# Kernel optimization log

Hardware: AMD Instinct MI355X
Metric: run time of the kernel (lower is better)

Reference implementation:

```python
import jax, jax.numpy as jnp
from jax import lax
import numpy as np

S, B, T = 512, 256, 128


def setup_inputs() -> dict:
    key = jax.random.key(0)
    k1, k2, k3, k4 = jax.random.split(key, 4)
    emissions = jax.random.normal(k1, (S, B, T), dtype=jnp.float32)
    mask = jnp.ones((S, B), dtype=jnp.int32)  # all positions valid
    start_transitions = jax.random.normal(k2, (T,), dtype=jnp.float32)
    end_transitions = jax.random.normal(k3, (T,), dtype=jnp.float32)
    transitions = jax.random.normal(k4, (T, T), dtype=jnp.float32)
    return {
        "emissions": emissions,
        "mask": mask,
        "start_transitions": start_transitions,
        "end_transitions": end_transitions,
        "transitions": transitions,
    }


def reference(emissions, mask, start_transitions, end_transitions, transitions):
    """Viterbi decode. emissions: [S,B,T], mask: [S,B].
    Returns (best_tags [B,S] int32, best_path_score [B] float32)."""
    seq_len, batch, num_tags = emissions.shape
    maskb = mask.astype(bool)

    score0 = start_transitions[None, :] + emissions[0]  # [B,T]

    def fwd_step(score, inp):
        em_t, m_t = inp  # [B,T], [B]
        # [B, T_prev, T_next]
        ns = score[:, :, None] + transitions[None, :, :] + em_t[:, None, :]
        next_score = ns.max(axis=1)          # [B,T]
        idx = ns.argmax(axis=1)              # [B,T] best previous tag
        score = jnp.where(m_t[:, None], next_score, score)
        return score, idx

    final_score, history = lax.scan(fwd_step, score0, (emissions[1:], maskb[1:]))
    final_score = final_score + end_transitions[None, :]

    best_last = jnp.argmax(final_score, axis=1)   # [B] tag at last valid position
    best_score = jnp.max(final_score, axis=1)     # [B]

    barange = jnp.arange(batch)

    def back_step(tag, inp):
        hist_t, m_t = inp  # [B,T], [B]
        prev = hist_t[barange, tag]
        tag = jnp.where(m_t, prev, tag)  # only follow history inside the sequence
        return tag, tag

    # reverse scan over transitions t -> t+1 for t = S-2 .. 0; ys[t] = tag at time t
    _, tags_prefix = lax.scan(back_step, best_last, (history, maskb[1:]), reverse=True)
    tags = jnp.concatenate([tags_prefix, best_last[None, :]], axis=0)  # [S,B]
    return tags.T.astype(jnp.int32), best_score
```

## Files before the change

kernel.cpp:

```cpp
#include <hip/hip_runtime.h>

#define SLEN  512
#define BATCH 256
#define NTAGS 128
#define NTHR  512

__device__ __forceinline__ int dpp_qperm_b1(int x) {
    return __builtin_amdgcn_update_dpp(0, x, 0xB1, 0xF, 0xF, true);
}
__device__ __forceinline__ int dpp_qperm_4e(int x) {
    return __builtin_amdgcn_update_dpp(0, x, 0x4E, 0xF, 0xF, true);
}

struct VI { float v; int i; };
__device__ __forceinline__ VI vmax2(VI a, VI b) { return (b.v > a.v) ? b : a; }

__global__ __launch_bounds__(NTHR, 2) void viterbi_kernel(
    const float* __restrict__ em,
    const int*   __restrict__ mask,
    const float* __restrict__ start_t,
    const float* __restrict__ end_t,
    const float* __restrict__ trans,
    float* __restrict__ out)
{
    const int b    = blockIdx.x;
    const int tid  = threadIdx.x;
    const int j    = tid >> 2;
    const int h    = tid & 3;
    const int base = h << 5;
    const bool writer = (h == 0);
    const int jslot = j + (j >> 5) * 8;

    __shared__ __align__(16) float scbuf[2][4 * 40];
    __shared__ float fin[NTAGS];
    __shared__ int   maskv[SLEN];
    __shared__ unsigned char hist[SLEN - 1][NTAGS];
    __shared__ unsigned char exitc[8][NTAGS];
    __shared__ unsigned char st_tags[8];
    __shared__ unsigned char tagseq[SLEN];
    __shared__ float bestval_s;
    __shared__ int   bestj_s;

    const float* trp = trans + (size_t)base * NTAGS + j;
    const float t00 = trp[ 0*NTAGS], t01 = trp[ 1*NTAGS], t02 = trp[ 2*NTAGS], t03 = trp[ 3*NTAGS];
    const float t04 = trp[ 4*NTAGS], t05 = trp[ 5*NTAGS], t06 = trp[ 6*NTAGS], t07 = trp[ 7*NTAGS];
    const float t08 = trp[ 8*NTAGS], t09 = trp[ 9*NTAGS], t10 = trp[10*NTAGS], t11 = trp[11*NTAGS];
    const float t12 = trp[12*NTAGS], t13 = trp[13*NTAGS], t14 = trp[14*NTAGS], t15 = trp[15*NTAGS];
    const float t16 = trp[16*NTAGS], t17 = trp[17*NTAGS], t18 = trp[18*NTAGS], t19 = trp[19*NTAGS];
    const float t20 = trp[20*NTAGS], t21 = trp[21*NTAGS], t22 = trp[22*NTAGS], t23 = trp[23*NTAGS];
    const float t24 = trp[24*NTAGS], t25 = trp[25*NTAGS], t26 = trp[26*NTAGS], t27 = trp[27*NTAGS];
    const float t28 = trp[28*NTAGS], t29 = trp[29*NTAGS], t30 = trp[30*NTAGS], t31 = trp[31*NTAGS];

    for (int t = tid; t < SLEN; t += NTHR)
        maskv[t] = mask[t * BATCH + b];

    float scj = 0.f;
    if (writer) {
        scj = start_t[j] + em[(size_t)b * NTAGS + j];
        scbuf[0][jslot] = scj;
    }
    __syncthreads();

    const float* emp = em + (size_t)BATCH * NTAGS + (size_t)b * NTAGS + j;
    float em_next = *emp;

    int p = 0;
    for (int t = 1; t < SLEN; ++t) {
        const float em_cur = em_next;
        if (t + 1 < SLEN) { emp += BATCH * NTAGS; em_next = *emp; }

        const float4* sq = (const float4*)&scbuf[p][h * 40];
        const float4 q0 = sq[0], q1 = sq[1], q2 = sq[2], q3 = sq[3];
        const float4 q4 = sq[4], q5 = sq[5], q6 = sq[6], q7 = sq[7];

        const float c00 = (q0.x + t00) + em_cur, c01 = (q0.y + t01) + em_cur;
        const float c02 = (q0.z + t02) + em_cur, c03 = (q0.w + t03) + em_cur;
        const float c04 = (q1.x + t04) + em_cur, c05 = (q1.y + t05) + em_cur;
        const float c06 = (q1.z + t06) + em_cur, c07 = (q1.w + t07) + em_cur;
        const float c08 = (q2.x + t08) + em_cur, c09 = (q2.y + t09) + em_cur;
        const float c10 = (q2.z + t10) + em_cur, c11 = (q2.w + t11) + em_cur;
        const float c12 = (q3.x + t12) + em_cur, c13 = (q3.y + t13) + em_cur;
        const float c14 = (q3.z + t14) + em_cur, c15 = (q3.w + t15) + em_cur;
        const float c16 = (q4.x + t16) + em_cur, c17 = (q4.y + t17) + em_cur;
        const float c18 = (q4.z + t18) + em_cur, c19 = (q4.w + t19) + em_cur;
        const float c20 = (q5.x + t20) + em_cur, c21 = (q5.y + t21) + em_cur;
        const float c22 = (q5.z + t22) + em_cur, c23 = (q5.w + t23) + em_cur;
        const float c24 = (q6.x + t24) + em_cur, c25 = (q6.y + t25) + em_cur;
        const float c26 = (q6.z + t26) + em_cur, c27 = (q6.w + t27) + em_cur;
        const float c28 = (q7.x + t28) + em_cur, c29 = (q7.y + t29) + em_cur;
        const float c30 = (q7.z + t30) + em_cur, c31 = (q7.w + t31) + em_cur;

        const VI m00 = vmax2(VI{c00, 0}, VI{c01, 1}),  m01 = vmax2(VI{c02, 2}, VI{c03, 3});
        const VI m02 = vmax2(VI{c04, 4}, VI{c05, 5}),  m03 = vmax2(VI{c06, 6}, VI{c07, 7});
        const VI m04 = vmax2(VI{c08, 8}, VI{c09, 9}),  m05 = vmax2(VI{c10,10}, VI{c11,11});
        const VI m06 = vmax2(VI{c12,12}, VI{c13,13}),  m07 = vmax2(VI{c14,14}, VI{c15,15});
        const VI m08 = vmax2(VI{c16,16}, VI{c17,17}),  m09 = vmax2(VI{c18,18}, VI{c19,19});
        const VI m10 = vmax2(VI{c20,20}, VI{c21,21}),  m11 = vmax2(VI{c22,22}, VI{c23,23});
        const VI m12 = vmax2(VI{c24,24}, VI{c25,25}),  m13 = vmax2(VI{c26,26}, VI{c27,27});
        const VI m14 = vmax2(VI{c28,28}, VI{c29,29}),  m15 = vmax2(VI{c30,30}, VI{c31,31});

        const VI n0 = vmax2(m00, m01), n1 = vmax2(m02, m03);
        const VI n2 = vmax2(m04, m05), n3 = vmax2(m06, m07);
        const VI n4 = vmax2(m08, m09), n5 = vmax2(m10, m11);
        const VI n6 = vmax2(m12, m13), n7 = vmax2(m14, m15);

        const VI o0 = vmax2(n0, n1), o1 = vmax2(n2, n3);
        const VI o2 = vmax2(n4, n5), o3 = vmax2(n6, n7);

        const VI p0 = vmax2(o0, o1), p1 = vmax2(o2, o3);
        const VI r  = vmax2(p0, p1);

        float v  = r.v;
        int   gi = base + r.i;
        {
            float vo = __int_as_float(dpp_qperm_b1(__float_as_int(v)));
            int   io = dpp_qperm_b1(gi);
            if (vo > v) { v = vo; gi = io; }
        }
        {
            float vo = __int_as_float(dpp_qperm_4e(__float_as_int(v)));
            int   io = dpp_qperm_4e(gi);
            if (vo > v) { v = vo; gi = io; }
        }

        if (writer) {
            hist[t - 1][j] = (unsigned char)gi;
            scj = maskv[t] ? v : scj;
            scbuf[p ^ 1][jslot] = scj;
        }
        __syncthreads();
        p ^= 1;
    }

    if (writer) fin[j] = scj + end_t[j];
    __syncthreads();

    if (tid < 64) {
        float v  = fin[tid]; int bj = tid;
        float v1 = fin[tid + 64];
        if (v1 > v) { v = v1; bj = tid + 64; }
#pragma unroll
        for (int off = 32; off > 0; off >>= 1) {
            float ov = __shfl_xor(v, off, 64);
            int   oj = __shfl_xor(bj, off, 64);
            if (ov > v || (ov == v && oj < bj)) { v = ov; bj = oj; }
        }
        if (tid == 0) { bestval_s = v; bestj_s = bj; }
    }
    __syncthreads();

    {
        const int k  = tid & 127;
        const int c0 = tid >> 7;
        const int c1 = c0 + 4;
        int tagA = k, tagB = k;
        for (int u = 63; u >= 0; --u) {
            const int sA = c0 * 64 + u;
            const int sB = c1 * 64 + u;
            if (sB <= SLEN - 2) {
                int pv = hist[sB][tagB];
                tagB = maskv[sB + 1] ? pv : tagB;
            }
            int pv = hist[sA][tagA];
            tagA = maskv[sA + 1] ? pv : tagA;
        }
        exitc[c0][k] = (unsigned char)tagA;
        exitc[c1][k] = (unsigned char)tagB;
    }
    __syncthreads();

    if (tid == 0) {
        int tag = bestj_s;
        for (int c = 7; c >= 0; --c) {
            st_tags[c] = (unsigned char)tag;
            tag = exitc[c][tag];
        }
        out[BATCH * SLEN + b] = bestval_s;
    }
    __syncthreads();

    if (tid < 8) {
        const int c = tid;
        int tag = st_tags[c];
        if (c == 7) tagseq[SLEN - 1] = (unsigned char)tag;
        const int shi = (c == 7) ? (SLEN - 2) : (c * 64 + 63);
        for (int s = shi; s >= c * 64; --s) {
            int pv = hist[s][tag];
            tag = maskv[s + 1] ? pv : tag;
            tagseq[s] = (unsigned char)tag;
        }
    }
    __syncthreads();

    out[b * SLEN + tid] = (float)tagseq[tid];
}

extern "C" void kernel_launch(void* const* d_in, const int* in_sizes, int n_in,
                              void* d_out, int out_size, void* d_ws, size_t ws_size,
                              hipStream_t stream) {
    const float* em      = (const float*)d_in[0];
    const int*   mask    = (const int*)d_in[1];
    const float* start_t = (const float*)d_in[2];
    const float* end_t   = (const float*)d_in[3];
    const float* trans   = (const float*)d_in[4];
    float* out = (float*)d_out;

    viterbi_kernel<<<dim3(BATCH), dim3(NTHR), 0, stream>>>(
        em, mask, start_t, end_t, trans, out);
}
```

Measured before the change: 405.7 us.

## Split each tag's max-reduction across eight lanes with 1024-thread blocks

Doubles the block size to 1024 threads so each next-tag column is reduced by 8 lanes over 16 previous tags instead of 4 lanes over 32. A third butterfly step using ds_swizzle xor-4 finishes the reduction, and the shared score buffer padding is changed to match. The backtrace chunk walk is rebalanced to one chunk per thread. The goal is a shorter per-step serial dependency chain and fewer transition registers per thread. In exchange it adds an extra cross-lane step and doubles the number of waves that must meet at the per-step barrier.

```diff
diff --git a/kernel.cpp b/kernel.cpp
--- a/kernel.cpp
+++ b/kernel.cpp
@@ -3,7 +3,7 @@
 #define SLEN  512
 #define BATCH 256
 #define NTAGS 128
-#define NTHR  512
+#define NTHR  1024
 
 __device__ __forceinline__ int dpp_qperm_b1(int x) {
     return __builtin_amdgcn_update_dpp(0, x, 0xB1, 0xF, 0xF, true);
@@ -11,11 +11,14 @@
 __device__ __forceinline__ int dpp_qperm_4e(int x) {
     return __builtin_amdgcn_update_dpp(0, x, 0x4E, 0xF, 0xF, true);
 }
+__device__ __forceinline__ int swz_xor4(int x) {
+    return __builtin_amdgcn_ds_swizzle(x, 0x101F);
+}
 
 struct VI { float v; int i; };
 __device__ __forceinline__ VI vmax2(VI a, VI b) { return (b.v > a.v) ? b : a; }
 
-__global__ __launch_bounds__(NTHR, 2) void viterbi_kernel(
+__global__ __launch_bounds__(NTHR, 4) void viterbi_kernel(
     const float* __restrict__ em,
     const int*   __restrict__ mask,
     const float* __restrict__ start_t,
@@ -25,13 +28,13 @@
 {
     const int b    = blockIdx.x;
     const int tid  = threadIdx.x;
-    const int j    = tid >> 2;
-    const int h    = tid & 3;
-    const int base = h << 5;
+    const int j    = tid >> 3;
+    const int h    = tid & 7;
+    const int base = h << 4;
     const bool writer = (h == 0);
-    const int jslot = j + (j >> 5) * 8;
+    const int jslot = j + (j >> 4) * 4;
 
-    __shared__ __align__(16) float scbuf[2][4 * 40];
+    __shared__ __align__(16) float scbuf[2][8 * 20];
     __shared__ float fin[NTAGS];
     __shared__ int   maskv[SLEN];
     __shared__ unsigned char hist[SLEN - 1][NTAGS];
@@ -46,13 +49,9 @@
     const float t04 = trp[ 4*NTAGS], t05 = trp[ 5*NTAGS], t06 = trp[ 6*NTAGS], t07 = trp[ 7*NTAGS];
     const float t08 = trp[ 8*NTAGS], t09 = trp[ 9*NTAGS], t10 = trp[10*NTAGS], t11 = trp[11*NTAGS];
     const float t12 = trp[12*NTAGS], t13 = trp[13*NTAGS], t14 = trp[14*NTAGS], t15 = trp[15*NTAGS];
-    const float t16 = trp[16*NTAGS], t17 = trp[17*NTAGS], t18 = trp[18*NTAGS], t19 = trp[19*NTAGS];
-    const float t20 = trp[20*NTAGS], t21 = trp[21*NTAGS], t22 = trp[22*NTAGS], t23 = trp[23*NTAGS];
-    const float t24 = trp[24*NTAGS], t25 = trp[25*NTAGS], t26 = trp[26*NTAGS], t27 = trp[27*NTAGS];
-    const float t28 = trp[28*NTAGS], t29 = trp[29*NTAGS], t30 = trp[30*NTAGS], t31 = trp[31*NTAGS];
 
-    for (int t = tid; t < SLEN; t += NTHR)
-        maskv[t] = mask[t * BATCH + b];
+    if (tid < SLEN)
+        maskv[tid] = mask[tid * BATCH + b];
 
     float scj = 0.f;
     if (writer) {
@@ -69,9 +68,8 @@
         const float em_cur = em_next;
         if (t + 1 < SLEN) { emp += BATCH * NTAGS; em_next = *emp; }
 
-        const float4* sq = (const float4*)&scbuf[p][h * 40];
+        const float4* sq = (const float4*)&scbuf[p][h * 20];
         const float4 q0 = sq[0], q1 = sq[1], q2 = sq[2], q3 = sq[3];
-        const float4 q4 = sq[4], q5 = sq[5], q6 = sq[6], q7 = sq[7];
 
         const float c00 = (q0.x + t00) + em_cur, c01 = (q0.y + t01) + em_cur;
         const float c02 = (q0.z + t02) + em_cur, c03 = (q0.w + t03) + em_cur;
@@ -81,34 +79,15 @@
         const float c10 = (q2.z + t10) + em_cur, c11 = (q2.w + t11) + em_cur;
         const float c12 = (q3.x + t12) + em_cur, c13 = (q3.y + t13) + em_cur;
         const float c14 = (q3.z + t14) + em_cur, c15 = (q3.w + t15) + em_cur;
-        const float c16 = (q4.x + t16) + em_cur, c17 = (q4.y + t17) + em_cur;
-        const float c18 = (q4.z + t18) + em_cur, c19 = (q4.w + t19) + em_cur;
-        const float c20 = (q5.x + t20) + em_cur, c21 = (q5.y + t21) + em_cur;
-        const float c22 = (q5.z + t22) + em_cur, c23 = (q5.w + t23) + em_cur;
-        const float c24 = (q6.x + t24) + em_cur, c25 = (q6.y + t25) + em_cur;
-        const float c26 = (q6.z + t26) + em_cur, c27 = (q6.w + t27) + em_cur;
-        const float c28 = (q7.x + t28) + em_cur, c29 = (q7.y + t29) + em_cur;
-        const float c30 = (q7.z + t30) + em_cur, c31 = (q7.w + t31) + em_cur;
 
-        const VI m00 = vmax2(VI{c00, 0}, VI{c01, 1}),  m01 = vmax2(VI{c02, 2}, VI{c03, 3});
-        const VI m02 = vmax2(VI{c04, 4}, VI{c05, 5}),  m03 = vmax2(VI{c06, 6}, VI{c07, 7});
-        const VI m04 = vmax2(VI{c08, 8}, VI{c09, 9}),  m05 = vmax2(VI{c10,10}, VI{c11,11});
-        const VI m06 = vmax2(VI{c12,12}, VI{c13,13}),  m07 = vmax2(VI{c14,14}, VI{c15,15});
-        const VI m08 = vmax2(VI{c16,16}, VI{c17,17}),  m09 = vmax2(VI{c18,18}, VI{c19,19});
-        const VI m10 = vmax2(VI{c20,20}, VI{c21,21}),  m11 = vmax2(VI{c22,22}, VI{c23,23});
-        const VI m12 = vmax2(VI{c24,24}, VI{c25,25}),  m13 = vmax2(VI{c26,26}, VI{c27,27});
-        const VI m14 = vmax2(VI{c28,28}, VI{c29,29}),  m15 = vmax2(VI{c30,30}, VI{c31,31});
-
-        const VI n0 = vmax2(m00, m01), n1 = vmax2(m02, m03);
-        const VI n2 = vmax2(m04, m05), n3 = vmax2(m06, m07);
-        const VI n4 = vmax2(m08, m09), n5 = vmax2(m10, m11);
-        const VI n6 = vmax2(m12, m13), n7 = vmax2(m14, m15);
-
+        const VI m0 = vmax2(VI{c00, 0}, VI{c01, 1}),  m1 = vmax2(VI{c02, 2}, VI{c03, 3});
+        const VI m2 = vmax2(VI{c04, 4}, VI{c05, 5}),  m3 = vmax2(VI{c06, 6}, VI{c07, 7});
+        const VI m4 = vmax2(VI{c08, 8}, VI{c09, 9}),  m5 = vmax2(VI{c10,10}, VI{c11,11});
+        const VI m6 = vmax2(VI{c12,12}, VI{c13,13}),  m7 = vmax2(VI{c14,14}, VI{c15,15});
+        const VI n0 = vmax2(m0, m1), n1 = vmax2(m2, m3);
+        const VI n2 = vmax2(m4, m5), n3 = vmax2(m6, m7);
         const VI o0 = vmax2(n0, n1), o1 = vmax2(n2, n3);
-        const VI o2 = vmax2(n4, n5), o3 = vmax2(n6, n7);
-
-        const VI p0 = vmax2(o0, o1), p1 = vmax2(o2, o3);
-        const VI r  = vmax2(p0, p1);
+        const VI r  = vmax2(o0, o1);
 
         float v  = r.v;
         int   gi = base + r.i;
@@ -120,6 +99,11 @@
         {
             float vo = __int_as_float(dpp_qperm_4e(__float_as_int(v)));
             int   io = dpp_qperm_4e(gi);
+            if (vo > v) { v = vo; gi = io; }
+        }
+        {
+            float vo = __int_as_float(swz_xor4(__float_as_int(v)));
+            int   io = swz_xor4(gi);
             if (vo > v) { v = vo; gi = io; }
         }
 
@@ -150,22 +134,17 @@
     __syncthreads();
 
     {
-        const int k  = tid & 127;
-        const int c0 = tid >> 7;
-        const int c1 = c0 + 4;
-        int tagA = k, tagB = k;
+        const int k = tid & 127;
+        const int c = tid >> 7;
+        int tag = k;
         for (int u = 63; u >= 0; --u) {
-            const int sA = c0 * 64 + u;
-            const int sB = c1 * 64 + u;
-            if (sB <= SLEN - 2) {
-                int pv = hist[sB][tagB];
-                tagB = maskv[sB + 1] ? pv : tagB;
+            const int s = c * 64 + u;
+            if (s <= SLEN - 2) {
+                int pv = hist[s][tag];
+                tag = maskv[s + 1] ? pv : tag;
             }
-            int pv = hist[sA][tagA];
-            tagA = maskv[sA + 1] ? pv : tagA;
         }
-        exitc[c0][k] = (unsigned char)tagA;
-        exitc[c1][k] = (unsigned char)tagB;
+        exitc[c][k] = (unsigned char)tag;
     }
     __syncthreads();
 
@@ -192,7 +171,8 @@
     }
     __syncthreads();
 
-    out[b * SLEN + tid] = (float)tagseq[tid];
+    if (tid < SLEN)
+        out[b * SLEN + tid] = (float)tagseq[tid];
 }
 
 extern "C" void kernel_launch(void* const* d_in, const int* in_sizes, int n_in,
```

Result: no change. 406.0 us (+0.1%).
